# Kernel tuning notes

Measured on AMD Instinct MI355X. Metric: run time of the kernel, lower is better.

## Reference

```python
import jax, jax.numpy as jnp
import numpy as np

N, E, F_IN, HID, OUT, HEADS, NG = 40000, 640000, 64, 128, 64, 4, 64
EPS = 1e-5

def setup_inputs() -> dict:
    key = jax.random.key(0)
    ks = jax.random.split(key, 32)
    d = {}
    d['x'] = jax.random.normal(ks[0], (N, F_IN), dtype=jnp.float32)
    d['edge_index'] = jax.random.randint(ks[1], (2, E), 0, N, dtype=jnp.int64)
    d['batch'] = jnp.sort(jax.random.randint(ks[2], (N,), 0, NG, dtype=jnp.int64))
    fins = [F_IN, HID, HID]
    for i in range(3):
        kk = jax.random.split(ks[3 + i], 6)
        fin = fins[i]
        d[f'W{i}'] = jax.random.normal(kk[0], (fin, HEADS * HID), dtype=jnp.float32) / np.sqrt(fin)
        d[f'as{i}'] = jax.random.normal(kk[1], (HEADS, HID), dtype=jnp.float32) / np.sqrt(HID)
        d[f'ad{i}'] = jax.random.normal(kk[2], (HEADS, HID), dtype=jnp.float32) / np.sqrt(HID)
        d[f'b{i}'] = jnp.zeros((HID,), dtype=jnp.float32)
        d[f'g{i}'] = jnp.ones((HID,), dtype=jnp.float32) + 0.05 * jax.random.normal(kk[3], (HID,), dtype=jnp.float32)
        d[f'be{i}'] = 0.05 * jax.random.normal(kk[4], (HID,), dtype=jnp.float32)
    d['fc1_w'] = jax.random.normal(ks[10], (HID, HID), dtype=jnp.float32) / np.sqrt(HID)
    d['fc1_b'] = jnp.zeros((HID,), dtype=jnp.float32)
    d['fc2_w'] = jax.random.normal(ks[11], (HID, OUT), dtype=jnp.float32) / np.sqrt(HID)
    d['fc2_b'] = jnp.zeros((OUT,), dtype=jnp.float32)
    return d

def _gat(x, src, dst, W, a_s, a_d, b):
    # PyG GATConv, heads=4, concat=False (mean over heads)
    xh = (x @ W).reshape(N, HEADS, HID)            # [N,H,C]
    s_src = jnp.einsum('nhc,hc->nh', xh, a_s)      # [N,H]
    s_dst = jnp.einsum('nhc,hc->nh', xh, a_d)
    e = jax.nn.leaky_relu(s_src[src] + s_dst[dst], 0.2)   # [Etot,H]
    m = jax.ops.segment_max(e, dst, num_segments=N)
    p = jnp.exp(e - m[dst])
    denom = jax.ops.segment_sum(p, dst, num_segments=N)
    alpha = p / denom[dst]                          # segment softmax over dst
    msg = xh[src] * alpha[:, :, None]               # [Etot,H,C]
    out = jax.ops.segment_sum(msg, dst, num_segments=N)  # [N,H,C]
    return out.mean(axis=1) + b

def _bn_eval(x, g, be):
    # running_mean=0, running_var=1 (eval mode)
    return x * (g / jnp.sqrt(1.0 + EPS)) + be

def reference(x, edge_index, batch, W0, as0, ad0, b0, g0, be0, W1, as1, ad1, b1, g1, be1, W2, as2, ad2, b2, g2, be2, fc1_w, fc1_b, fc2_w, fc2_b):
    loop = jnp.arange(N, dtype=edge_index.dtype)
    src = jnp.concatenate([edge_index[0], loop])   # add_self_loops (PyG default)
    dst = jnp.concatenate([edge_index[1], loop])
    h = x
    params = [(W0, as0, ad0, b0, g0, be0), (W1, as1, ad1, b1, g1, be1), (W2, as2, ad2, b2, g2, be2)]
    for (W, a_s, a_d, b, g, be) in params:
        h = _gat(h, src, dst, W, a_s, a_d, b)
        h = jax.nn.relu(_bn_eval(h, g, be))
        # dropout is identity in eval mode
    sums = jax.ops.segment_sum(h, batch, num_segments=NG)
    cnt = jax.ops.segment_sum(jnp.ones((N,), h.dtype), batch, num_segments=NG)
    pooled = sums / jnp.maximum(cnt, 1.0)[:, None]   # global_mean_pool [NG,HID]
    out = jax.nn.relu(pooled @ fc1_w + fc1_b)
    return out @ fc2_w + fc2_b
```

## Files before the change

### kernel.cpp

```cpp
#include <hip/hip_runtime.h>
#include <hip/hip_fp16.h>
#include <math.h>

#define N_NODES 40000
#define N_EDGES 640000
#define FIN 64
#define HID 128
#define OUTDIM 64
#define HEADS 4
#define NGROUPS 64
#define NCOLS 512

typedef _Float16 half8 __attribute__((ext_vector_type(8)));
typedef float f32x4 __attribute__((ext_vector_type(4)));

__device__ __forceinline__ float lrelu(float x) { return x > 0.f ? x : 0.2f * x; }

#define PREP_X4   (N_NODES * FIN / 4)
#define PREP_WSWZ 20480
#define PREP_V    2560
__global__ void prep_kernel(const float* __restrict__ x, __half* __restrict__ x16,
                            const float* __restrict__ W0, const float* __restrict__ W1,
                            const float* __restrict__ W2,
                            _Float16* __restrict__ F0, _Float16* __restrict__ F1,
                            _Float16* __restrict__ F2,
                            const float* __restrict__ as0, const float* __restrict__ ad0,
                            const float* __restrict__ as1, const float* __restrict__ ad1,
                            const float* __restrict__ as2, const float* __restrict__ ad2,
                            float* __restrict__ v0, float* __restrict__ v1,
                            float* __restrict__ v2) {
    int id = blockIdx.x * 256 + threadIdx.x;
    if (id < PREP_X4) {
        int i4 = id * 4;
        float4 v = *(const float4*)(x + i4);
        __half2 a = __floats2half2_rn(v.x, v.y);
        __half2 b = __floats2half2_rn(v.z, v.w);
        *(__half2*)(x16 + i4)     = a;
        *(__half2*)(x16 + i4 + 2) = b;
        return;
    }
    id -= PREP_X4;
    if (id < PREP_WSWZ) {
        const float* W; _Float16* F; int Kin;
        if (id < 4096)       { W = W0; F = F0; Kin = FIN; }
        else if (id < 12288) { W = W1; F = F1; Kin = HID; id -= 4096; }
        else                 { W = W2; F = F2; Kin = HID; id -= 12288; }
        int KP = Kin * 4;
        int NKg = KP / 32;
        int lane = id & 63;
        int blob = id >> 6;
        int k0g = blob % NKg;
        int cb  = blob / NKg;
        int col = cb * 16 + (lane & 15);
        int kkb = k0g * 32 + (lane >> 4) * 8;
        half8 v;
        #pragma unroll
        for (int e = 0; e < 8; ++e) {
            int kk = kkb + e;
            int k = kk & (Kin - 1);
            int h = kk / Kin;
            v[e] = (_Float16)(0.25f * W[(size_t)k * NCOLS + h * HID + col]);
        }
        *(half8*)(F + (size_t)blob * 512 + lane * 8) = v;
        return;
    }
    id -= PREP_WSWZ;
    if (id < PREP_V) {
        const float* W; const float* as_; const float* ad_; float* v; int j = id;
        if (j < FIN * 8)              { W = W0; as_ = as0; ad_ = ad0; v = v0; }
        else if (j < (FIN + HID) * 8) { W = W1; as_ = as1; ad_ = ad1; v = v1; j -= FIN * 8; }
        else                          { W = W2; as_ = as2; ad_ = ad2; v = v2; j -= (FIN + HID) * 8; }
        int k = j >> 3, sd = (j >> 2) & 1, h = j & 3;
        const float* av = sd ? ad_ : as_;
        float acc = 0.f;
        for (int c = 0; c < HID; ++c)
            acc += W[(size_t)k * NCOLS + h * HID + c] * av[h * HID + c];
        v[k * 8 + sd * 4 + h] = acc;
    }
}

__global__ void deg_count_kernel(const int* __restrict__ ei, int* deg) {
    int e = blockIdx.x * blockDim.x + threadIdx.x;
    if (e < N_EDGES) atomicAdd(&deg[ei[N_EDGES + e]], 1);
}

__global__ void scan1_kernel(const int* __restrict__ deg, int* offsets, int* partial) {
    __shared__ int buf[256];
    int t = threadIdx.x;
    int i = blockIdx.x * 256 + t;
    int v = (i < N_NODES) ? deg[i] + 1 : 0;
    buf[t] = v;
    __syncthreads();
    for (int off = 1; off < 256; off <<= 1) {
        int y = (t >= off) ? buf[t - off] : 0;
        __syncthreads();
        buf[t] += y;
        __syncthreads();
    }
    if (i < N_NODES) offsets[i] = buf[t] - v;
    if (t == 255) partial[blockIdx.x] = buf[255];
}

__global__ void scan2_kernel(int* partial, int nb) {
    __shared__ int buf[256];
    int t = threadIdx.x;
    int v = (t < nb) ? partial[t] : 0;
    buf[t] = v;
    __syncthreads();
    for (int off = 1; off < 256; off <<= 1) {
        int y = (t >= off) ? buf[t - off] : 0;
        __syncthreads();
        buf[t] += y;
        __syncthreads();
    }
    if (t < nb) partial[t] = buf[t] - v;
}

__global__ void scan3_kernel(int* offsets, int* pos, const int* __restrict__ partial) {
    int i = blockIdx.x * 256 + threadIdx.x;
    if (i < N_NODES) {
        int o = offsets[i] + partial[i >> 8];
        offsets[i] = o;
        pos[i] = o;
    }
    if (i == 0) offsets[N_NODES] = N_EDGES + N_NODES;
}

__global__ void scatter_kernel(const int* __restrict__ ei, int* pos,
                               int* csr_src, int* csr_dst) {
    int i = blockIdx.x * blockDim.x + threadIdx.x;
    if (i < N_EDGES) {
        int s = ei[i];
        int d = ei[N_EDGES + i];
        int p = atomicAdd(&pos[d], 1);
        csr_src[p] = s;
        csr_dst[p] = d;
    } else if (i < N_EDGES + N_NODES) {
        int nn = i - N_EDGES;
        int p = atomicAdd(&pos[nn], 1);
        csr_src[p] = nn;
        csr_dst[p] = nn;
    }
}

template <int K>
__global__ __launch_bounds__(256) void scores3_kernel(const __half* __restrict__ x,
                                                      const float* __restrict__ v,
                                                      float* __restrict__ ssrc,
                                                      float* __restrict__ sdst) {
    __shared__ float vs[K * 8];
    int t = threadIdx.x;
    for (int i = t; i < K * 8; i += 256) vs[i] = v[i];
    __syncthreads();
    int node = blockIdx.x * 256 + t;
    if (node >= N_NODES) return;
    const __half* xr = x + (size_t)node * K;
    f32x4 as = {0.f, 0.f, 0.f, 0.f};
    f32x4 ad = {0.f, 0.f, 0.f, 0.f};
    #pragma unroll 4
    for (int k0 = 0; k0 < K; k0 += 8) {
        uint4 u = *(const uint4*)(xr + k0);
        __half2* hp = (__half2*)&u;
        #pragma unroll
        for (int q = 0; q < 4; ++q) {
            float2 f = __half22float2(hp[q]);
            int k = k0 + 2 * q;
            as += f.x * *(const f32x4*)&vs[k * 8];
            ad += f.x * *(const f32x4*)&vs[k * 8 + 4];
            as += f.y * *(const f32x4*)&vs[(k + 1) * 8];
            ad += f.y * *(const f32x4*)&vs[(k + 1) * 8 + 4];
        }
    }
    *(f32x4*)(ssrc + node * 4) = as;
    *(f32x4*)(sdst + node * 4) = ad;
}

__global__ __launch_bounds__(256) void edge_val_kernel(const float* __restrict__ ssrc,
                                                       const float* __restrict__ sdst,
                                                       const int* __restrict__ csr_src,
                                                       const int* __restrict__ csr_dst,
                                                       float* __restrict__ val) {
    int j = blockIdx.x * 256 + threadIdx.x;
    if (j >= N_EDGES + N_NODES) return;
    int s = csr_src[j], d = csr_dst[j];
    float4 a = *(const float4*)(ssrc + s * 4);
    float4 b = *(const float4*)(sdst + d * 4);
    float4 v;
    v.x = __expf(lrelu(a.x + b.x));
    v.y = __expf(lrelu(a.y + b.y));
    v.z = __expf(lrelu(a.z + b.z));
    v.w = __expf(lrelu(a.w + b.w));
    *(float4*)(val + (size_t)j * 4) = v;
}

template <int K, bool SCORES>
__global__ __launch_bounds__(512) void fused_layer_kernel(
        const __half* __restrict__ tab16,
        const float* __restrict__ val,
        const int* __restrict__ offsets,
        const int* __restrict__ csr_src,
        const _Float16* __restrict__ Wf,
        const float* __restrict__ bias,
        const float* __restrict__ gamma,
        const float* __restrict__ beta,
        const float* __restrict__ vtab_next,
        __half* __restrict__ h16out,
        float* __restrict__ ssrc_o,
        float* __restrict__ sdst_o) {
    constexpr int KP = 4 * K;
    constexpr int EPR = (K == 128) ? 4 : 8;
    constexpr int LPE = 64 / EPR;
    constexpr int NKg = KP / 32;

    __shared__ _Float16 As[32][KP + 8];
    __shared__ float bn_s[3][HID];
    __shared__ float vs[SCORES ? HID * 8 : 8];
    _Float16 (*tb)[136] = (_Float16(*)[136])&As[0][0];

    int t = threadIdx.x;
    int lane = t & 63;
    int wv = t >> 6;
    int bm = blockIdx.x * 32;

    if (t < HID) {
        bn_s[0][t] = bias[t];
        bn_s[1][t] = gamma[t] * rsqrtf(1.f + 1e-5f);
        bn_s[2][t] = beta[t];
    }
    if (SCORES)
        for (int i = t; i < HID * 8; i += 512) vs[i] = vtab_next[i];

    int cgrp = lane & (LPE - 1);
    int egoff = lane / LPE;
    const char* xb = (const char*)tab16 + cgrp * 16;

    for (int i = 0; i < 4; ++i) {
        int nl = wv * 4 + i;
        int n = bm + nl;
        int start = offsets[n], end = offsets[n + 1];
        int deg = end - start;
        float acc[4][8] = {};
        f32x4 dsum = {0.f, 0.f, 0.f, 0.f};

        int j = 0;
        for (; j + 2 * EPR <= deg; j += 2 * EPR) {
            int egA = start + j + egoff;
            int egB = egA + EPR;
            int srcA = csr_src[egA];
            int srcB = csr_src[egB];
            float4 vA = *(const float4*)(val + (size_t)egA * 4);
            float4 vB = *(const float4*)(val + (size_t)egB * 4);
            uint4 uA = *(const uint4*)(xb + (uint)srcA * (K * 2));
            uint4 uB = *(const uint4*)(xb + (uint)srcB * (K * 2));
            f32x4 aA = {vA.x, vA.y, vA.z, vA.w};
            f32x4 aB = {vB.x, vB.y, vB.z, vB.w};
            dsum += aA;
            dsum += aB;
            __half2* hA = (__half2*)&uA;
            __half2* hB = (__half2*)&uB;
            #pragma unroll
            for (int q = 0; q < 4; ++q) {
                float2 fA = __half22float2(hA[q]);
                float2 fB = __half22float2(hB[q]);
                #pragma unroll
                for (int h = 0; h < 4; ++h) {
                    acc[h][2 * q]     += aA[h] * fA.x + aB[h] * fB.x;
                    acc[h][2 * q + 1] += aA[h] * fA.y + aB[h] * fB.y;
                }
            }
        }
        for (; j < deg; j += EPR) {
            int eg = j + egoff;
            bool act = eg < deg;
            int ec = act ? eg : deg - 1;
            int src = csr_src[start + ec];
            float4 vv = *(const float4*)(val + (size_t)(start + ec) * 4);
            f32x4 a4;
            a4[0] = act ? vv.x : 0.f;
            a4[1] = act ? vv.y : 0.f;
            a4[2] = act ? vv.z : 0.f;
            a4[3] = act ? vv.w : 0.f;
            dsum += a4;
            uint4 u = *(const uint4*)(xb + (uint)src * (K * 2));
            __half2* hp = (__half2*)&u;
            #pragma unroll
            for (int q = 0; q < 4; ++q) {
                float2 f = __half22float2(hp[q]);
                #pragma unroll
                for (int h = 0; h < 4; ++h) {
                    acc[h][2 * q]     += a4[h] * f.x;
                    acc[h][2 * q + 1] += a4[h] * f.y;
                }
            }
        }

        #pragma unroll
        for (int stride = LPE; stride < 64; stride <<= 1) {
            #pragma unroll
            for (int h = 0; h < 4; ++h) {
                #pragma unroll
                for (int r = 0; r < 8; ++r)
                    acc[h][r] += __shfl_xor(acc[h][r], stride);
                dsum[h] += __shfl_xor(dsum[h], stride);
            }
        }
        if (lane < LPE) {
            #pragma unroll
            for (int h = 0; h < 4; ++h) {
                float inv = 1.f / dsum[h];
                half8 v;
                #pragma unroll
                for (int r = 0; r < 8; ++r) v[r] = (_Float16)(acc[h][r] * inv);
                *(half8*)&As[nl][h * K + cgrp * 8] = v;
            }
        }
    }
    __syncthreads();

    int wm = wv >> 2, wn = wv & 3;
    int lr = lane & 15;
    int lk = (lane >> 4) * 8;
    int lg = lane >> 4;
    f32x4 acc2[2] = {};
    #pragma unroll
    for (int k0g = 0; k0g < NKg; ++k0g) {
        half8 af = *(const half8*)&As[wm * 16 + lr][k0g * 32 + lk];
        #pragma unroll
        for (int nn = 0; nn < 2; ++nn) {
            int cb = wn * 2 + nn;
            half8 bf = *(const half8*)(Wf + ((size_t)(cb * NKg + k0g) << 9) + lane * 8);
            acc2[nn] = __builtin_amdgcn_mfma_f32_16x16x32_f16(af, bf, acc2[nn], 0, 0, 0);
        }
    }
    __syncthreads();

    #pragma unroll
    for (int nn = 0; nn < 2; ++nn) {
        int col = wn * 32 + nn * 16 + lr;
        float b = bn_s[0][col], g = bn_s[1][col], be = bn_s[2][col];
        #pragma unroll
        for (int r = 0; r < 4; ++r) {
            float o = acc2[nn][r] + b;
            o = o * g + be;
            tb[wm * 16 + lg * 4 + r][col] = (_Float16)fmaxf(o, 0.f);
        }
    }
    __syncthreads();

    {
        int row = t >> 4;
        int c0 = (t & 15) * 8;
        half8 v0 = *(const half8*)&tb[row][c0];
        *(half8*)((_Float16*)h16out + (size_t)(bm + row) * HID + c0) = v0;
    }

    if (SCORES) {
        if (t < 256) {
            int node = t >> 3, j = t & 7;
            float sacc = 0.f;
            #pragma unroll 2
            for (int k0 = 0; k0 < HID; k0 += 8) {
                half8 hv = *(const half8*)&tb[node][k0];
                #pragma unroll
                for (int e = 0; e < 8; ++e)
                    sacc += (float)hv[e] * vs[(k0 + e) * 8 + j];
            }
            if (j < 4) ssrc_o[(bm + node) * 4 + j] = sacc;
            else       sdst_o[(bm + node) * 4 + (j - 4)] = sacc;
        }
    }
}

__global__ __launch_bounds__(128) void pool_kernel(const __half* __restrict__ h,
                                                   const int* __restrict__ batch,
                                                   float* pooled, float* counts) {
    int t = threadIdx.x;
    int which = t >> 6;
    int c2 = (t & 63) * 2;
    int n0 = blockIdx.x * 256 + which;
    int n1 = min(blockIdx.x * 256 + 256, N_NODES);
    if (n0 >= N_NODES) return;
    int cg = batch[n0];
    float a0 = 0.f, a1 = 0.f, cnt = 0.f;
    for (int n = n0; n < n1; n += 2) {
        int g = batch[n];
        if (g != cg) {
            atomicAdd(&pooled[cg * HID + c2], a0);
            atomicAdd(&pooled[cg * HID + c2 + 1], a1);
            if ((t & 63) == 0) atomicAdd(&counts[cg], cnt);
            a0 = 0.f; a1 = 0.f; cnt = 0.f; cg = g;
        }
        uint u = *(const uint*)(h + (size_t)n * HID + c2);
        __half2 hh = *(__half2*)&u;
        float2 f = __half22float2(hh);
        a0 += f.x; a1 += f.y; cnt += 1.f;
    }
    atomicAdd(&pooled[cg * HID + c2], a0);
    atomicAdd(&pooled[cg * HID + c2 + 1], a1);
    if ((t & 63) == 0) atomicAdd(&counts[cg], cnt);
}

__global__ __launch_bounds__(128) void head_kernel(const float* __restrict__ pooled,
                                                   const float* __restrict__ counts,
                                                   const float* __restrict__ fc1_w,
                                                   const float* __restrict__ fc1_b,
                                                   const float* __restrict__ fc2_w,
                                                   const float* __restrict__ fc2_b,
                                                   float* __restrict__ out) {
    int gI = blockIdx.x;
    int t = threadIdx.x;
    __shared__ float p[HID], hb[HID];
    p[t] = pooled[gI * HID + t] / fmaxf(counts[gI], 1.f);
    __syncthreads();
    float a = fc1_b[t];
    #pragma unroll 4
    for (int k = 0; k < HID; ++k) a += p[k] * fc1_w[k * HID + t];
    hb[t] = fmaxf(a, 0.f);
    __syncthreads();
    if (t < OUTDIM) {
        float o = fc2_b[t];
        #pragma unroll 4
        for (int k = 0; k < HID; ++k) o += hb[k] * fc2_w[k * OUTDIM + t];
        out[gI * OUTDIM + t] = o;
    }
}

extern "C" void kernel_launch(void* const* d_in, const int* in_sizes, int n_in,
                              void* d_out, int out_size, void* d_ws, size_t ws_size,
                              hipStream_t stream) {
    const float* x     = (const float*)d_in[0];
    const int*   ei    = (const int*)d_in[1];
    const int*   batch = (const int*)d_in[2];
    const float* W[3]  = {(const float*)d_in[3],  (const float*)d_in[9],  (const float*)d_in[15]};
    const float* As_[3] = {(const float*)d_in[4],  (const float*)d_in[10], (const float*)d_in[16]};
    const float* Ad[3] = {(const float*)d_in[5],  (const float*)d_in[11], (const float*)d_in[17]};
    const float* Bb[3] = {(const float*)d_in[6],  (const float*)d_in[12], (const float*)d_in[18]};
    const float* Gg[3] = {(const float*)d_in[7],  (const float*)d_in[13], (const float*)d_in[19]};
    const float* Be[3] = {(const float*)d_in[8],  (const float*)d_in[14], (const float*)d_in[20]};
    const float* fc1_w = (const float*)d_in[21];
    const float* fc1_b = (const float*)d_in[22];
    const float* fc2_w = (const float*)d_in[23];
    const float* fc2_b = (const float*)d_in[24];

    char* ws = (char*)d_ws;
    size_t off = 0;
    auto alloc = [&](size_t bytes) {
        void* p = ws + off;
        off = (off + bytes + 255) & ~(size_t)255;
        return p;
    };
    __half* x16    = (__half*)alloc((size_t)N_NODES * FIN * 2);
    __half* h16A   = (__half*)alloc((size_t)N_NODES * HID * 2);
    __half* h16B   = (__half*)alloc((size_t)N_NODES * HID * 2);
    _Float16* Wf[3];
    Wf[0] = (_Float16*)alloc((size_t)(4 * FIN) * HID * 2);
    Wf[1] = (_Float16*)alloc((size_t)(4 * HID) * HID * 2);
    Wf[2] = (_Float16*)alloc((size_t)(4 * HID) * HID * 2);
    float* vtab[3];
    vtab[0] = (float*)alloc((size_t)FIN * 8 * 4);
    vtab[1] = (float*)alloc((size_t)HID * 8 * 4);
    vtab[2] = (float*)alloc((size_t)HID * 8 * 4);
    float* ssrcA   = (float*)alloc((size_t)N_NODES * HEADS * 4);
    float* sdstA   = (float*)alloc((size_t)N_NODES * HEADS * 4);
    float* ssrcB   = (float*)alloc((size_t)N_NODES * HEADS * 4);
    float* sdstB   = (float*)alloc((size_t)N_NODES * HEADS * 4);
    float* val     = (float*)alloc((size_t)(N_EDGES + N_NODES) * 4 * 4);
    int*   deg     = (int*)alloc((size_t)N_NODES * 4);
    int*   offsets = (int*)alloc((size_t)(N_NODES + 1) * 4);
    int*   pos     = (int*)alloc((size_t)N_NODES * 4);
    int*   partial = (int*)alloc((size_t)256 * 4);
    int*   csr     = (int*)alloc((size_t)(N_EDGES + N_NODES) * 4);
    int*   csrd    = (int*)alloc((size_t)(N_EDGES + N_NODES) * 4);
    float* pooled  = (float*)alloc((size_t)NGROUPS * HID * 4 + (size_t)NGROUPS * 4);
    float* counts  = pooled + (size_t)NGROUPS * HID;

    const int PREP_TOTAL = PREP_X4 + PREP_WSWZ + PREP_V;
    prep_kernel<<<(PREP_TOTAL + 255) / 256, 256, 0, stream>>>(
        x, x16, W[0], W[1], W[2], Wf[0], Wf[1], Wf[2],
        As_[0], Ad[0], As_[1], Ad[1], As_[2], Ad[2], vtab[0], vtab[1], vtab[2]);

    const int NB = (N_NODES + 255) / 256;
    hipMemsetAsync(deg, 0, (size_t)N_NODES * 4, stream);
    deg_count_kernel<<<(N_EDGES + 255) / 256, 256, 0, stream>>>(ei, deg);
    scan1_kernel<<<NB, 256, 0, stream>>>(deg, offsets, partial);
    scan2_kernel<<<1, 256, 0, stream>>>(partial, NB);
    scan3_kernel<<<NB, 256, 0, stream>>>(offsets, pos, partial);
    scatter_kernel<<<(N_EDGES + N_NODES + 255) / 256, 256, 0, stream>>>(ei, pos, csr, csrd);

    const int EB = (N_EDGES + N_NODES + 255) / 256;

    scores3_kernel<64><<<NB, 256, 0, stream>>>(x16, vtab[0], ssrcA, sdstA);

    edge_val_kernel<<<EB, 256, 0, stream>>>(ssrcA, sdstA, csr, csrd, val);
    fused_layer_kernel<64, true><<<N_NODES / 32, 512, 0, stream>>>(
        x16, val, offsets, csr, Wf[0], Bb[0], Gg[0], Be[0],
        vtab[1], h16A, ssrcB, sdstB);
    edge_val_kernel<<<EB, 256, 0, stream>>>(ssrcB, sdstB, csr, csrd, val);
    fused_layer_kernel<128, true><<<N_NODES / 32, 512, 0, stream>>>(
        h16A, val, offsets, csr, Wf[1], Bb[1], Gg[1], Be[1],
        vtab[2], h16B, ssrcA, sdstA);
    edge_val_kernel<<<EB, 256, 0, stream>>>(ssrcA, sdstA, csr, csrd, val);
    fused_layer_kernel<128, false><<<N_NODES / 32, 512, 0, stream>>>(
        h16B, val, offsets, csr, Wf[2], Bb[2], Gg[2], Be[2],
        nullptr, h16A, nullptr, nullptr);

    hipMemsetAsync(pooled, 0, (size_t)NGROUPS * HID * 4 + (size_t)NGROUPS * 4, stream);
    pool_kernel<<<(N_NODES + 255) / 256, 128, 0, stream>>>(h16A, batch, pooled, counts);
    head_kernel<<<NGROUPS, 128, 0, stream>>>(pooled, counts, fc1_w, fc1_b, fc2_w, fc2_b,
                                             (float*)d_out);
}
```

Before: 370.4 us.

## Fuse edge attention exp computation into aggregation kernel, drop val buffer

Removes the separate edge_val kernel that materialized per-edge exp(leaky_relu(s_src+s_dst)) into a large buffer for each layer. The fused layer kernel now gathers s_src per source node and computes the exponent inline, using the destination score loaded once per node. This also drops the csr_dst array and its writes in scatter. It also adds an occupancy hint to launch_bounds. The cost is recomputing exp in each lane group, since every lane in a group redoes the same edge's four exps, plus an extra random gather of s_src.

```diff
diff --git a/kernel.cpp b/kernel.cpp
--- a/kernel.cpp
+++ b/kernel.cpp
@@ -126,20 +126,15 @@
     if (i == 0) offsets[N_NODES] = N_EDGES + N_NODES;
 }
 
-__global__ void scatter_kernel(const int* __restrict__ ei, int* pos,
-                               int* csr_src, int* csr_dst) {
+__global__ void scatter_kernel(const int* __restrict__ ei, int* pos, int* csr_src) {
     int i = blockIdx.x * blockDim.x + threadIdx.x;
     if (i < N_EDGES) {
         int s = ei[i];
         int d = ei[N_EDGES + i];
-        int p = atomicAdd(&pos[d], 1);
-        csr_src[p] = s;
-        csr_dst[p] = d;
+        csr_src[atomicAdd(&pos[d], 1)] = s;
     } else if (i < N_EDGES + N_NODES) {
         int nn = i - N_EDGES;
-        int p = atomicAdd(&pos[nn], 1);
-        csr_src[p] = nn;
-        csr_dst[p] = nn;
+        csr_src[atomicAdd(&pos[nn], 1)] = nn;
     }
 }
 
@@ -175,28 +170,11 @@
     *(f32x4*)(sdst + node * 4) = ad;
 }
 
-__global__ __launch_bounds__(256) void edge_val_kernel(const float* __restrict__ ssrc,
-                                                       const float* __restrict__ sdst,
-                                                       const int* __restrict__ csr_src,
-                                                       const int* __restrict__ csr_dst,
-                                                       float* __restrict__ val) {
-    int j = blockIdx.x * 256 + threadIdx.x;
-    if (j >= N_EDGES + N_NODES) return;
-    int s = csr_src[j], d = csr_dst[j];
-    float4 a = *(const float4*)(ssrc + s * 4);
-    float4 b = *(const float4*)(sdst + d * 4);
-    float4 v;
-    v.x = __expf(lrelu(a.x + b.x));
-    v.y = __expf(lrelu(a.y + b.y));
-    v.z = __expf(lrelu(a.z + b.z));
-    v.w = __expf(lrelu(a.w + b.w));
-    *(float4*)(val + (size_t)j * 4) = v;
-}
-
 template <int K, bool SCORES>
-__global__ __launch_bounds__(512) void fused_layer_kernel(
+__global__ __launch_bounds__(512, 8) void fused_layer_kernel(
         const __half* __restrict__ tab16,
-        const float* __restrict__ val,
+        const float* __restrict__ s_src,
+        const float* __restrict__ s_dst,
         const int* __restrict__ offsets,
         const int* __restrict__ csr_src,
         const _Float16* __restrict__ Wf,
@@ -239,6 +217,7 @@
         int n = bm + nl;
         int start = offsets[n], end = offsets[n + 1];
         int deg = end - start;
+        const float4 sd = *(const float4*)(s_dst + n * 4);
         float acc[4][8] = {};
         f32x4 dsum = {0.f, 0.f, 0.f, 0.f};
 
@@ -248,12 +227,19 @@
             int egB = egA + EPR;
             int srcA = csr_src[egA];
             int srcB = csr_src[egB];
-            float4 vA = *(const float4*)(val + (size_t)egA * 4);
-            float4 vB = *(const float4*)(val + (size_t)egB * 4);
+            float4 qA = *(const float4*)(s_src + srcA * 4);
+            float4 qB = *(const float4*)(s_src + srcB * 4);
             uint4 uA = *(const uint4*)(xb + (uint)srcA * (K * 2));
             uint4 uB = *(const uint4*)(xb + (uint)srcB * (K * 2));
-            f32x4 aA = {vA.x, vA.y, vA.z, vA.w};
-            f32x4 aB = {vB.x, vB.y, vB.z, vB.w};
+            f32x4 aA, aB;
+            aA[0] = __expf(lrelu(qA.x + sd.x));
+            aA[1] = __expf(lrelu(qA.y + sd.y));
+            aA[2] = __expf(lrelu(qA.z + sd.z));
+            aA[3] = __expf(lrelu(qA.w + sd.w));
+            aB[0] = __expf(lrelu(qB.x + sd.x));
+            aB[1] = __expf(lrelu(qB.y + sd.y));
+            aB[2] = __expf(lrelu(qB.z + sd.z));
+            aB[3] = __expf(lrelu(qB.w + sd.w));
             dsum += aA;
             dsum += aB;
             __half2* hA = (__half2*)&uA;
@@ -274,12 +260,12 @@
             bool act = eg < deg;
             int ec = act ? eg : deg - 1;
             int src = csr_src[start + ec];
-            float4 vv = *(const float4*)(val + (size_t)(start + ec) * 4);
+            float4 qq = *(const float4*)(s_src + src * 4);
             f32x4 a4;
-            a4[0] = act ? vv.x : 0.f;
-            a4[1] = act ? vv.y : 0.f;
-            a4[2] = act ? vv.z : 0.f;
-            a4[3] = act ? vv.w : 0.f;
+            a4[0] = act ? __expf(lrelu(qq.x + sd.x)) : 0.f;
+            a4[1] = act ? __expf(lrelu(qq.y + sd.y)) : 0.f;
+            a4[2] = act ? __expf(lrelu(qq.z + sd.z)) : 0.f;
+            a4[3] = act ? __expf(lrelu(qq.w + sd.w)) : 0.f;
             dsum += a4;
             uint4 u = *(const uint4*)(xb + (uint)src * (K * 2));
             __half2* hp = (__half2*)&u;
@@ -464,13 +450,11 @@
     float* sdstA   = (float*)alloc((size_t)N_NODES * HEADS * 4);
     float* ssrcB   = (float*)alloc((size_t)N_NODES * HEADS * 4);
     float* sdstB   = (float*)alloc((size_t)N_NODES * HEADS * 4);
-    float* val     = (float*)alloc((size_t)(N_EDGES + N_NODES) * 4 * 4);
     int*   deg     = (int*)alloc((size_t)N_NODES * 4);
     int*   offsets = (int*)alloc((size_t)(N_NODES + 1) * 4);
     int*   pos     = (int*)alloc((size_t)N_NODES * 4);
     int*   partial = (int*)alloc((size_t)256 * 4);
     int*   csr     = (int*)alloc((size_t)(N_EDGES + N_NODES) * 4);
-    int*   csrd    = (int*)alloc((size_t)(N_EDGES + N_NODES) * 4);
     float* pooled  = (float*)alloc((size_t)NGROUPS * HID * 4 + (size_t)NGROUPS * 4);
     float* counts  = pooled + (size_t)NGROUPS * HID;
 
@@ -485,23 +469,18 @@
     scan1_kernel<<<NB, 256, 0, stream>>>(deg, offsets, partial);
     scan2_kernel<<<1, 256, 0, stream>>>(partial, NB);
     scan3_kernel<<<NB, 256, 0, stream>>>(offsets, pos, partial);
-    scatter_kernel<<<(N_EDGES + N_NODES + 255) / 256, 256, 0, stream>>>(ei, pos, csr, csrd);
-
-    const int EB = (N_EDGES + N_NODES + 255) / 256;
+    scatter_kernel<<<(N_EDGES + N_NODES + 255) / 256, 256, 0, stream>>>(ei, pos, csr);
 
     scores3_kernel<64><<<NB, 256, 0, stream>>>(x16, vtab[0], ssrcA, sdstA);
 
-    edge_val_kernel<<<EB, 256, 0, stream>>>(ssrcA, sdstA, csr, csrd, val);
     fused_layer_kernel<64, true><<<N_NODES / 32, 512, 0, stream>>>(
-        x16, val, offsets, csr, Wf[0], Bb[0], Gg[0], Be[0],
+        x16, ssrcA, sdstA, offsets, csr, Wf[0], Bb[0], Gg[0], Be[0],
         vtab[1], h16A, ssrcB, sdstB);
-    edge_val_kernel<<<EB, 256, 0, stream>>>(ssrcB, sdstB, csr, csrd, val);
     fused_layer_kernel<128, true><<<N_NODES / 32, 512, 0, stream>>>(
-        h16A, val, offsets, csr, Wf[1], Bb[1], Gg[1], Be[1],
+        h16A, ssrcB, sdstB, offsets, csr, Wf[1], Bb[1], Gg[1], Be[1],
         vtab[2], h16B, ssrcA, sdstA);
-    edge_val_kernel<<<EB, 256, 0, stream>>>(ssrcA, sdstA, csr, csrd, val);
     fused_layer_kernel<128, false><<<N_NODES / 32, 512, 0, stream>>>(
-        h16B, val, offsets, csr, Wf[2], Bb[2], Gg[2], Be[2],
+        h16B, ssrcA, sdstA, offsets, csr, Wf[2], Bb[2], Gg[2], Be[2],
         nullptr, h16A, nullptr, nullptr);
 
     hipMemsetAsync(pooled, 0, (size_t)NGROUPS * HID * 4 + (size_t)NGROUPS * 4, stream);
```

Result: slower. 572.6 us (+54.6%).
